# Performance work log

Measured on AMD Instinct MI355X. Metric: run time of the kernel, lower is better.

Reference implementation:

```python
import jax, jax.numpy as jnp
import numpy as np

N_NODES = 200000
N_EDGES = 6400000
NUM_GRAPHS = 20000
D_NODE, D_EDGE, D_MSG = 5, 4, 10


def setup_inputs() -> dict:
    key = jax.random.key(0)
    ks = jax.random.split(key, 16)
    inp = {
        "edge_index": jax.random.randint(ks[0], (2, N_EDGES), 0, N_NODES, dtype=jnp.int64)
                      if jax.config.jax_enable_x64 else
                      jax.random.randint(ks[0], (2, N_EDGES), 0, N_NODES, dtype=jnp.int32),
        "node_attr": jax.random.normal(ks[1], (N_NODES, D_NODE), dtype=jnp.float32),
        "edge_attr": jax.random.normal(ks[2], (N_EDGES, D_EDGE), dtype=jnp.float32),
        "batch": jnp.sort(jax.random.randint(ks[3], (N_NODES,), 0, NUM_GRAPHS, dtype=jnp.int32)),
        "num_graphs": NUM_GRAPHS,
        # MPL_1: Linear(2*D_NODE + D_EDGE -> 10)
        "w_mpl": jax.random.normal(ks[4], (2 * D_NODE + D_EDGE, D_MSG), dtype=jnp.float32) * 0.3,
        "b_mpl": jnp.zeros((D_MSG,), dtype=jnp.float32),
        "w1": jax.random.normal(ks[5], (10, 10), dtype=jnp.float32) * 0.3,
        "b1": jnp.zeros((10,), dtype=jnp.float32),
        "w2": jax.random.normal(ks[6], (10, 5), dtype=jnp.float32) * 0.3,
        "b2": jnp.zeros((5,), dtype=jnp.float32),
        "w3": jax.random.normal(ks[7], (5, 5), dtype=jnp.float32) * 0.3,
        "b3": jnp.zeros((5,), dtype=jnp.float32),
        "w4": jax.random.normal(ks[8], (5, 1), dtype=jnp.float32) * 0.3,
        "b4": jnp.zeros((1,), dtype=jnp.float32),
    }
    return inp


def reference(edge_index, node_attr, edge_attr, batch, num_graphs,
              w_mpl, b_mpl, w1, b1, w2, b2, w3, b3, w4, b4):
    src, dst = edge_index[0], edge_index[1]
    n_nodes = node_attr.shape[0]
    # MPL_1: gather endpoints, concat with edge features, MLP, scatter-sum to dst
    edge_in = jnp.concatenate(
        [node_attr[src], node_attr[dst], edge_attr], axis=-1)  # [E, 14]
    msg = jax.nn.relu(edge_in @ w_mpl + b_mpl)                 # [E, 10]
    x = jax.ops.segment_sum(msg, dst, num_segments=n_nodes)    # [N, 10]
    # node MLP head
    x = jax.nn.relu(x @ w1 + b1)
    x = jax.nn.relu(x @ w2 + b2)
    # segment_coo(reduce='sum') over sorted batch index -> per-graph pooling
    x = jax.ops.segment_sum(x, batch, num_segments=num_graphs,
                            indices_are_sorted=True)           # [G, 5]
    x = jax.nn.relu(x @ w3 + b3)
    return x @ w4 + b4                                         # [G, 1]
```

## Files before the change

### kernel.cpp

```cpp
#include <hip/hip_runtime.h>
#include <hip/hip_fp16.h>

#define DN 5
#define DE 4
#define DM 10
#define NB 2048
#define BKT_SH 8
#define BKT_NODES 256
#define MAXBKT 1024

#define PERM(b) (((b) & 7) * (NB / 8) + ((b) >> 3))

typedef float        f4  __attribute__((ext_vector_type(4)));
typedef unsigned int u4v __attribute__((ext_vector_type(4)));

static __device__ __forceinline__ float2 h2f(unsigned u) {
    __half2 h = *reinterpret_cast<__half2*>(&u);
    return make_float2(__low2float(h), __high2float(h));
}
static __device__ __forceinline__ unsigned f2h(float a, float b) {
    __half2 h = __floats2half2_rn(a, b);
    return *reinterpret_cast<unsigned*>(&h);
}

__global__ __launch_bounds__(256) void hist_pack_kernel(
    const int* __restrict__ ei, const float* __restrict__ node_attr,
    u4v* __restrict__ naph, unsigned* __restrict__ cnt,
    int E, int chunk, int nbk, int N)
{
    __shared__ unsigned hist[MAXBKT];
    int t = threadIdx.x, b = blockIdx.x;

    int n = b * 256 + t;
    if (n < N) {
        const float* r = node_attr + (size_t)n * DN;
        u4v v;
        v.x = f2h(r[0], r[1]);
        v.y = f2h(r[2], r[3]);
        v.z = f2h(r[4], 0.f);
        v.w = 0u;
        naph[n] = v;
    }

    for (int j = t; j < nbk; j += 256) hist[j] = 0;
    __syncthreads();

    int e0 = b * chunk, e1 = min(E, e0 + chunk);
    for (int i = e0 + t; i < e1; i += 256) {
        int d = __builtin_nontemporal_load(ei + (size_t)E + i);
        atomicAdd(&hist[d >> BKT_SH], 1u);
    }
    __syncthreads();
    for (int j = t; j < nbk; j += 256)
        cnt[(size_t)j * NB + PERM(b)] = hist[j];
}

__global__ __launch_bounds__(256) void scan_rows_kernel(
    unsigned* __restrict__ cnt, unsigned* __restrict__ rowtotal)
{
    __shared__ unsigned lds[256];
    int j = blockIdx.x, t = threadIdx.x;
    unsigned* row = cnt + (size_t)j * NB;

    unsigned v[8], s = 0;
#pragma unroll
    for (int u = 0; u < 8; ++u) { v[u] = row[t * 8 + u]; s += v[u]; }
    lds[t] = s; __syncthreads();
#pragma unroll
    for (int o = 1; o < 256; o <<= 1) {
        unsigned add = (t >= o) ? lds[t - o] : 0u;
        __syncthreads();
        lds[t] += add;
        __syncthreads();
    }
    unsigned excl = lds[t] - s;
#pragma unroll
    for (int u = 0; u < 8; ++u) { row[t * 8 + u] = excl; excl += v[u]; }
    if (t == 255) rowtotal[j] = lds[255];
}

__global__ __launch_bounds__(1024) void scan_base_kernel(
    const unsigned* __restrict__ rowtotal, unsigned* __restrict__ gbase,
    int nbk, int E)
{
    __shared__ unsigned lds[1024];
    int t = threadIdx.x;
    unsigned v = (t < nbk) ? rowtotal[t] : 0u;
    lds[t] = v; __syncthreads();
#pragma unroll
    for (int o = 1; o < 1024; o <<= 1) {
        unsigned add = (t >= o) ? lds[t - o] : 0u;
        __syncthreads();
        lds[t] += add;
        __syncthreads();
    }
    unsigned excl = lds[t] - v;
    if (t < nbk)       gbase[t] = excl;
    else if (t == nbk) gbase[t] = (unsigned)E;
}

__global__ __launch_bounds__(256) void scatter_kernel(
    const int* __restrict__ ei, const float* __restrict__ edge_attr,
    const unsigned* __restrict__ cnt, const unsigned* __restrict__ gbase,
    const u4v* __restrict__ naph,
    f4* __restrict__ rec, int E, int chunk, int nbk)
{
    __shared__ unsigned woff[MAXBKT];
    int t = threadIdx.x, b = blockIdx.x;
    for (int j = t; j < nbk; j += 256)
        woff[j] = gbase[j] + cnt[(size_t)j * NB + PERM(b)];
    __syncthreads();

    int e0 = b * chunk, e1 = min(E, e0 + chunk);
    for (int i0 = e0 + t; i0 < e1; i0 += 4 * 256) {
        int s[4], d[4]; f4 ea[4]; bool act[4];
#pragma unroll
        for (int u = 0; u < 4; ++u) {
            int i = i0 + u * 256;
            act[u] = (i < e1);
            if (act[u]) {
                s[u]  = __builtin_nontemporal_load(ei + i);
                d[u]  = __builtin_nontemporal_load(ei + (size_t)E + i);
                ea[u] = __builtin_nontemporal_load(
                            reinterpret_cast<const f4*>(edge_attr) + i);
            }
        }
        u4v nap[4];
#pragma unroll
        for (int u = 0; u < 4; ++u)
            if (act[u]) nap[u] = naph[s[u]];
#pragma unroll
        for (int u = 0; u < 4; ++u) {
            if (!act[u]) continue;
            unsigned p = atomicAdd(&woff[d[u] >> BKT_SH], 1u);
            f4 r0, r1;
            r0.x = __uint_as_float((unsigned)(d[u] & 255));
            r0.y = __uint_as_float(nap[u].x);
            r0.z = __uint_as_float(nap[u].y);
            r0.w = __uint_as_float(nap[u].z);
            r1.x = __uint_as_float(f2h(ea[u].x, ea[u].y));
            r1.y = __uint_as_float(f2h(ea[u].z, ea[u].w));
            r1.z = 0.f; r1.w = 0.f;
            rec[2 * (size_t)p]     = r0;
            rec[2 * (size_t)p + 1] = r1;
        }
    }
}

__global__ __launch_bounds__(256) void gather_kernel(
    const f4* __restrict__ rec, const unsigned* __restrict__ gbase,
    const u4v* __restrict__ naph,
    const float* __restrict__ w_mpl, const float* __restrict__ b_mpl,
    float* __restrict__ xpart, size_t xstride,
    int E, int N, int nbk, int nsplit)
{
    __shared__ float acc[BKT_NODES * DM];
    __shared__ float pdl[BKT_NODES * 12];
    __shared__ float sws[50];
    __shared__ float swe[40];

    int t = threadIdx.x;
    int j  = blockIdx.x / nsplit;
    int sp = blockIdx.x - j * nsplit;
    int nb0 = j * BKT_NODES;

    if (t < 50)       sws[t] = w_mpl[t];
    else if (t < 90)  swe[t - 50] = w_mpl[100 + (t - 50)];

    for (int i = t; i < BKT_NODES * DM; i += 256) acc[i] = 0.f;

    {
        int n = nb0 + t;
        float a0 = 0.f, a1 = 0.f, a2 = 0.f, a3 = 0.f, a4 = 0.f;
        if (n < N) {
            u4v v = naph[n];
            float2 p01 = h2f(v.x), p23 = h2f(v.y), p4 = h2f(v.z);
            a0 = p01.x; a1 = p01.y; a2 = p23.x; a3 = p23.y; a4 = p4.x;
        }
#pragma unroll
        for (int q = 0; q < DM; ++q) {
            float v = b_mpl[q];
            v = fmaf(a0, w_mpl[50 + q], v);
            v = fmaf(a1, w_mpl[60 + q], v);
            v = fmaf(a2, w_mpl[70 + q], v);
            v = fmaf(a3, w_mpl[80 + q], v);
            v = fmaf(a4, w_mpl[90 + q], v);
            pdl[t * 12 + q] = v;
        }
    }
    __syncthreads();

    unsigned start = gbase[j];
    unsigned end   = gbase[j + 1];
    unsigned blen  = end - start;
    unsigned csz   = (blen + nsplit - 1) / nsplit;
    unsigned ss    = start + (unsigned)sp * csz;
    unsigned se    = min(end, ss + csz);

    for (unsigned i0 = ss + t; i0 < se; i0 += 4u * 256u) {
        f4 r0[4], r1[4]; bool act[4];
#pragma unroll
        for (int u = 0; u < 4; ++u) {
            unsigned i = i0 + (unsigned)u * 256u;
            act[u] = (i < se);
            if (act[u]) {
                r0[u] = __builtin_nontemporal_load(rec + 2 * (size_t)i);
                r1[u] = __builtin_nontemporal_load(rec + 2 * (size_t)i + 1);
            }
        }
#pragma unroll
        for (int u = 0; u < 4; ++u) {
            if (!act[u]) continue;
            int dl = (int)__float_as_uint(r0[u].x);
            float2 s01 = h2f(__float_as_uint(r0[u].y));
            float2 s23 = h2f(__float_as_uint(r0[u].z));
            float2 s4_ = h2f(__float_as_uint(r0[u].w));
            float2 e01 = h2f(__float_as_uint(r1[u].x));
            float2 e23 = h2f(__float_as_uint(r1[u].y));
            float a0 = s01.x, a1 = s01.y, a2 = s23.x, a3 = s23.y, a4 = s4_.x;
            float e0 = e01.x, e1 = e01.y, e2 = e23.x, e3 = e23.y;

            const float* pr = &pdl[dl * 12];
            float4 p0 = *reinterpret_cast<const float4*>(pr);
            float4 p1 = *reinterpret_cast<const float4*>(pr + 4);
            float2 p2 = *reinterpret_cast<const float2*>(pr + 8);
            float m[DM] = {p0.x, p0.y, p0.z, p0.w, p1.x, p1.y, p1.z, p1.w, p2.x, p2.y};
#pragma unroll
            for (int q = 0; q < DM; ++q) {
                float v = m[q];
                v = fmaf(a0, sws[q],      v);
                v = fmaf(a1, sws[10 + q], v);
                v = fmaf(a2, sws[20 + q], v);
                v = fmaf(a3, sws[30 + q], v);
                v = fmaf(a4, sws[40 + q], v);
                v = fmaf(e0, swe[q],      v);
                v = fmaf(e1, swe[10 + q], v);
                v = fmaf(e2, swe[20 + q], v);
                v = fmaf(e3, swe[30 + q], v);
                if (v > 0.f) atomicAdd(&acc[dl * DM + q], v);
            }
        }
    }
    __syncthreads();

    float* dst = xpart + (size_t)sp * xstride + (size_t)nb0 * DM;
    for (int i = t; i < BKT_NODES * DM; i += 256)
        __builtin_nontemporal_store(acc[i], dst + i);
}

__global__ __launch_bounds__(256) void combine_kernel(
    const float* __restrict__ xpart, size_t xstride,
    const int* __restrict__ batch,
    const float* __restrict__ w1, const float* __restrict__ b1,
    const float* __restrict__ w2, const float* __restrict__ b2,
    float* __restrict__ gacc, int N, int nsplit)
{
    __shared__ float s1[100], sb1[10], s2[50], sb2[5];
    int t = threadIdx.x;
    if (t < 100)      s1[t] = w1[t];
    else if (t < 110) sb1[t - 100] = b1[t - 100];
    else if (t < 160) s2[t - 110] = w2[t - 110];
    else if (t < 165) sb2[t - 160] = b2[t - 160];
    __syncthreads();

    int n = blockIdx.x * blockDim.x + t;
    bool valid = (n < N);
    int g = 0x7fffffff;
    float h2[5] = {0.f, 0.f, 0.f, 0.f, 0.f};

    if (valid) {
        float x[DM];
#pragma unroll
        for (int q = 0; q < DM; ++q) x[q] = 0.f;
        for (int sp = 0; sp < nsplit; ++sp) {
            const float2* row = reinterpret_cast<const float2*>(
                xpart + (size_t)sp * xstride + (size_t)n * DM);
#pragma unroll
            for (int h = 0; h < 5; ++h) {
                float2 v = row[h];
                x[2 * h] += v.x; x[2 * h + 1] += v.y;
            }
        }

        float h1[10];
#pragma unroll
        for (int q = 0; q < 10; ++q) h1[q] = sb1[q];
#pragma unroll
        for (int k = 0; k < 10; ++k)
#pragma unroll
            for (int q = 0; q < 10; ++q) h1[q] = fmaf(x[k], s1[k * 10 + q], h1[q]);
#pragma unroll
        for (int q = 0; q < 10; ++q) h1[q] = fmaxf(h1[q], 0.f);
#pragma unroll
        for (int q = 0; q < 5; ++q) h2[q] = sb2[q];
#pragma unroll
        for (int k = 0; k < 10; ++k)
#pragma unroll
            for (int q = 0; q < 5; ++q) h2[q] = fmaf(h1[k], s2[k * 5 + q], h2[q]);
#pragma unroll
        for (int q = 0; q < 5; ++q) h2[q] = fmaxf(h2[q], 0.f);
        g = batch[n];
    }

    int lane = t & 63;
#pragma unroll
    for (int o = 1; o < 64; o <<= 1) {
        int go = __shfl_down(g, o);
        float v0 = __shfl_down(h2[0], o);
        float v1 = __shfl_down(h2[1], o);
        float v2 = __shfl_down(h2[2], o);
        float v3 = __shfl_down(h2[3], o);
        float v4 = __shfl_down(h2[4], o);
        if (lane + o < 64 && go == g) {
            h2[0] += v0; h2[1] += v1; h2[2] += v2; h2[3] += v3; h2[4] += v4;
        }
    }
    int gp = __shfl_up(g, 1);
    bool head = (lane == 0) || (gp != g);
    if (head && g != 0x7fffffff) {
#pragma unroll
        for (int q = 0; q < 5; ++q)
            if (h2[q] != 0.f) unsafeAtomicAdd(&gacc[(size_t)g * 5 + q], h2[q]);
    }
}

__global__ __launch_bounds__(256) void graph_head_kernel(
    const float* __restrict__ gacc,
    const float* __restrict__ w3, const float* __restrict__ b3,
    const float* __restrict__ w4, const float* __restrict__ b4,
    float* __restrict__ out, int G)
{
    __shared__ float s3[25], sb3[5], s4[5], sb4[1];
    int t = threadIdx.x;
    if (t < 25)       s3[t] = w3[t];
    else if (t < 30)  sb3[t - 25] = b3[t - 25];
    else if (t < 35)  s4[t - 30] = w4[t - 30];
    else if (t == 35) sb4[0] = b4[0];
    __syncthreads();

    int g = blockIdx.x * blockDim.x + t;
    if (g >= G) return;

    float x[5];
#pragma unroll
    for (int k = 0; k < 5; ++k) x[k] = gacc[(size_t)g * 5 + k];

    float o = sb4[0];
#pragma unroll
    for (int q = 0; q < 5; ++q) {
        float h = sb3[q];
#pragma unroll
        for (int k = 0; k < 5; ++k) h = fmaf(x[k], s3[k * 5 + q], h);
        h = fmaxf(h, 0.f);
        o = fmaf(h, s4[q], o);
    }
    out[g] = o;
}

extern "C" void kernel_launch(void* const* d_in, const int* in_sizes, int n_in,
                              void* d_out, int out_size, void* d_ws, size_t ws_size,
                              hipStream_t stream)
{
    const int*   ei        = (const int*)d_in[0];
    const float* node_attr = (const float*)d_in[1];
    const float* edge_attr = (const float*)d_in[2];
    const int*   batch     = (const int*)d_in[3];
    const float* w_mpl = (const float*)d_in[5];
    const float* b_mpl = (const float*)d_in[6];
    const float* w1    = (const float*)d_in[7];
    const float* b1    = (const float*)d_in[8];
    const float* w2    = (const float*)d_in[9];
    const float* b2    = (const float*)d_in[10];
    const float* w3    = (const float*)d_in[11];
    const float* b3    = (const float*)d_in[12];
    const float* w4    = (const float*)d_in[13];
    const float* b4    = (const float*)d_in[14];
    float* out = (float*)d_out;

    const int E = in_sizes[0] / 2;
    const int N = in_sizes[1] / DN;
    const int G = out_size;

    const int nbk   = (N + BKT_NODES - 1) / BKT_NODES;
    const int chunk = (E + NB - 1) / NB;

    char* p = (char*)d_ws;
    f4*       rec      = (f4*)p;       p += (size_t)E * 32;
    u4v*      naph     = (u4v*)p;      p += (size_t)N * 16;
    unsigned* rowtotal = (unsigned*)p; p += ((size_t)nbk * 4 + 15) & ~15ull;
    unsigned* gbase    = (unsigned*)p; p += ((size_t)(nbk + 1) * 4 + 15) & ~15ull;
    float*    gacc     = (float*)p;    p += (size_t)G * 5 * 4;
    unsigned* cnt      = (unsigned*)p;
    float*    xpart    = (float*)p;
    size_t cnt_bytes = (size_t)nbk * NB * 4;

    size_t used = (size_t)((char*)cnt - (char*)d_ws);
    size_t xstride = (size_t)nbk * BKT_NODES * DM;
    int nsplit = 8;
    while (nsplit > 1 &&
           used + ((cnt_bytes > (size_t)nsplit * xstride * 4) ? cnt_bytes
                                                              : (size_t)nsplit * xstride * 4) > ws_size)
        nsplit >>= 1;

    hipMemsetAsync(gacc, 0, (size_t)G * 5 * 4, stream);

    hist_pack_kernel<<<NB, 256, 0, stream>>>(ei, node_attr, naph, cnt, E, chunk, nbk, N);
    scan_rows_kernel<<<nbk, 256, 0, stream>>>(cnt, rowtotal);
    scan_base_kernel<<<1, 1024, 0, stream>>>(rowtotal, gbase, nbk, E);
    scatter_kernel<<<NB, 256, 0, stream>>>(ei, edge_attr, cnt, gbase, naph, rec, E, chunk, nbk);
    gather_kernel<<<nbk * nsplit, 256, 0, stream>>>(rec, gbase, naph, w_mpl, b_mpl,
                                                    xpart, xstride, E, N, nbk, nsplit);
    combine_kernel<<<nbk, 256, 0, stream>>>(xpart, xstride, batch, w1, b1, w2, b2, gacc, N, nsplit);
    graph_head_kernel<<<(G + 255) / 256, 256, 0, stream>>>(gacc, w3, b3, w4, b4, out, G);
}
```

Measured before the change: 587.0 us.

## Shrink edge records to 16 bytes and gather source features in gather kernel

The scatter pass now writes a single 16-byte record per edge: the source index and local destination bits packed into one word, plus the half-precision edge features. It no longer writes a 32-byte record holding the prefetched fp16 source node features. The gather kernel instead does a random lookup into the packed node feature table using the source index. This halves record write and read traffic but moves a random 16-byte gather from the scatter stage into the gather stage. It also assumes node indices fit in 18 bits.

```diff
diff --git a/kernel.cpp b/kernel.cpp
--- a/kernel.cpp
+++ b/kernel.cpp
@@ -102,8 +102,7 @@
 __global__ __launch_bounds__(256) void scatter_kernel(
     const int* __restrict__ ei, const float* __restrict__ edge_attr,
     const unsigned* __restrict__ cnt, const unsigned* __restrict__ gbase,
-    const u4v* __restrict__ naph,
-    f4* __restrict__ rec, int E, int chunk, int nbk)
+    u4v* __restrict__ rec, int E, int chunk, int nbk)
 {
     __shared__ unsigned woff[MAXBKT];
     int t = threadIdx.x, b = blockIdx.x;
@@ -125,30 +124,22 @@
                             reinterpret_cast<const f4*>(edge_attr) + i);
             }
         }
-        u4v nap[4];
-#pragma unroll
-        for (int u = 0; u < 4; ++u)
-            if (act[u]) nap[u] = naph[s[u]];
 #pragma unroll
         for (int u = 0; u < 4; ++u) {
             if (!act[u]) continue;
             unsigned p = atomicAdd(&woff[d[u] >> BKT_SH], 1u);
-            f4 r0, r1;
-            r0.x = __uint_as_float((unsigned)(d[u] & 255));
-            r0.y = __uint_as_float(nap[u].x);
-            r0.z = __uint_as_float(nap[u].y);
-            r0.w = __uint_as_float(nap[u].z);
-            r1.x = __uint_as_float(f2h(ea[u].x, ea[u].y));
-            r1.y = __uint_as_float(f2h(ea[u].z, ea[u].w));
-            r1.z = 0.f; r1.w = 0.f;
-            rec[2 * (size_t)p]     = r0;
-            rec[2 * (size_t)p + 1] = r1;
+            u4v r;
+            r.x = (unsigned)s[u] | ((unsigned)(d[u] & 255) << 18);
+            r.y = f2h(ea[u].x, ea[u].y);
+            r.z = f2h(ea[u].z, ea[u].w);
+            r.w = 0u;
+            rec[p] = r;
         }
     }
 }
 
 __global__ __launch_bounds__(256) void gather_kernel(
-    const f4* __restrict__ rec, const unsigned* __restrict__ gbase,
+    const u4v* __restrict__ rec, const unsigned* __restrict__ gbase,
     const u4v* __restrict__ naph,
     const float* __restrict__ w_mpl, const float* __restrict__ b_mpl,
     float* __restrict__ xpart, size_t xstride,
@@ -198,25 +189,26 @@
     unsigned se    = min(end, ss + csz);
 
     for (unsigned i0 = ss + t; i0 < se; i0 += 4u * 256u) {
-        f4 r0[4], r1[4]; bool act[4];
+        u4v r[4]; bool act[4];
 #pragma unroll
         for (int u = 0; u < 4; ++u) {
             unsigned i = i0 + (unsigned)u * 256u;
             act[u] = (i < se);
-            if (act[u]) {
-                r0[u] = __builtin_nontemporal_load(rec + 2 * (size_t)i);
-                r1[u] = __builtin_nontemporal_load(rec + 2 * (size_t)i + 1);
-            }
-        }
+            if (act[u]) r[u] = __builtin_nontemporal_load(rec + i);
+        }
+        u4v nap[4];
+#pragma unroll
+        for (int u = 0; u < 4; ++u)
+            if (act[u]) nap[u] = naph[r[u].x & 0x3FFFFu];
 #pragma unroll
         for (int u = 0; u < 4; ++u) {
             if (!act[u]) continue;
-            int dl = (int)__float_as_uint(r0[u].x);
-            float2 s01 = h2f(__float_as_uint(r0[u].y));
-            float2 s23 = h2f(__float_as_uint(r0[u].z));
-            float2 s4_ = h2f(__float_as_uint(r0[u].w));
-            float2 e01 = h2f(__float_as_uint(r1[u].x));
-            float2 e23 = h2f(__float_as_uint(r1[u].y));
+            int dl = (int)((r[u].x >> 18) & 255u);
+            float2 s01 = h2f(nap[u].x);
+            float2 s23 = h2f(nap[u].y);
+            float2 s4_ = h2f(nap[u].z);
+            float2 e01 = h2f(r[u].y);
+            float2 e23 = h2f(r[u].z);
             float a0 = s01.x, a1 = s01.y, a2 = s23.x, a3 = s23.y, a4 = s4_.x;
             float e0 = e01.x, e1 = e01.y, e2 = e23.x, e3 = e23.y;
 
@@ -266,7 +258,7 @@
     int n = blockIdx.x * blockDim.x + t;
     bool valid = (n < N);
     int g = 0x7fffffff;
-    float h2[5] = {0.f, 0.f, 0.f, 0.f, 0.f};
+    float h2v[5] = {0.f, 0.f, 0.f, 0.f, 0.f};
 
     if (valid) {
         float x[DM];
@@ -292,13 +284,13 @@
 #pragma unroll
         for (int q = 0; q < 10; ++q) h1[q] = fmaxf(h1[q], 0.f);
 #pragma unroll
-        for (int q = 0; q < 5; ++q) h2[q] = sb2[q];
+        for (int q = 0; q < 5; ++q) h2v[q] = sb2[q];
 #pragma unroll
         for (int k = 0; k < 10; ++k)
 #pragma unroll
-            for (int q = 0; q < 5; ++q) h2[q] = fmaf(h1[k], s2[k * 5 + q], h2[q]);
-#pragma unroll
-        for (int q = 0; q < 5; ++q) h2[q] = fmaxf(h2[q], 0.f);
+            for (int q = 0; q < 5; ++q) h2v[q] = fmaf(h1[k], s2[k * 5 + q], h2v[q]);
+#pragma unroll
+        for (int q = 0; q < 5; ++q) h2v[q] = fmaxf(h2v[q], 0.f);
         g = batch[n];
     }
 
@@ -306,13 +298,13 @@
 #pragma unroll
     for (int o = 1; o < 64; o <<= 1) {
         int go = __shfl_down(g, o);
-        float v0 = __shfl_down(h2[0], o);
-        float v1 = __shfl_down(h2[1], o);
-        float v2 = __shfl_down(h2[2], o);
-        float v3 = __shfl_down(h2[3], o);
-        float v4 = __shfl_down(h2[4], o);
+        float v0 = __shfl_down(h2v[0], o);
+        float v1 = __shfl_down(h2v[1], o);
+        float v2 = __shfl_down(h2v[2], o);
+        float v3 = __shfl_down(h2v[3], o);
+        float v4 = __shfl_down(h2v[4], o);
         if (lane + o < 64 && go == g) {
-            h2[0] += v0; h2[1] += v1; h2[2] += v2; h2[3] += v3; h2[4] += v4;
+            h2v[0] += v0; h2v[1] += v1; h2v[2] += v2; h2v[3] += v3; h2v[4] += v4;
         }
     }
     int gp = __shfl_up(g, 1);
@@ -320,7 +312,7 @@
     if (head && g != 0x7fffffff) {
 #pragma unroll
         for (int q = 0; q < 5; ++q)
-            if (h2[q] != 0.f) unsafeAtomicAdd(&gacc[(size_t)g * 5 + q], h2[q]);
+            if (h2v[q] != 0.f) unsafeAtomicAdd(&gacc[(size_t)g * 5 + q], h2v[q]);
     }
 }
 
@@ -385,7 +377,7 @@
     const int chunk = (E + NB - 1) / NB;
 
     char* p = (char*)d_ws;
-    f4*       rec      = (f4*)p;       p += (size_t)E * 32;
+    u4v*      rec      = (u4v*)p;      p += (size_t)E * 16;
     u4v*      naph     = (u4v*)p;      p += (size_t)N * 16;
     unsigned* rowtotal = (unsigned*)p; p += ((size_t)nbk * 4 + 15) & ~15ull;
     unsigned* gbase    = (unsigned*)p; p += ((size_t)(nbk + 1) * 4 + 15) & ~15ull;
@@ -407,7 +399,7 @@
     hist_pack_kernel<<<NB, 256, 0, stream>>>(ei, node_attr, naph, cnt, E, chunk, nbk, N);
     scan_rows_kernel<<<nbk, 256, 0, stream>>>(cnt, rowtotal);
     scan_base_kernel<<<1, 1024, 0, stream>>>(rowtotal, gbase, nbk, E);
-    scatter_kernel<<<NB, 256, 0, stream>>>(ei, edge_attr, cnt, gbase, naph, rec, E, chunk, nbk);
+    scatter_kernel<<<NB, 256, 0, stream>>>(ei, edge_attr, cnt, gbase, rec, E, chunk, nbk);
     gather_kernel<<<nbk * nsplit, 256, 0, stream>>>(rec, gbase, naph, w_mpl, b_mpl,
                                                     xpart, xstride, E, N, nbk, nsplit);
     combine_kernel<<<nbk, 256, 0, stream>>>(xpart, xstride, batch, w1, b1, w2, b2, gacc, N, nsplit);
```

Result: faster. 506.4 us (-13.7%).
